# Optimization experiments

Hardware: AMD Instinct MI355X
Metric: run time of the kernel (lower is better)

The kernel has to match this reference:

```python
import jax, jax.numpy as jnp
import numpy as np

N_NODES = 25000
N_EDGES = 400000
EMBED_DIM = 128
NUM_HEADS = 8
D_K = EMBED_DIM // NUM_HEADS


def setup_inputs() -> dict:
    key = jax.random.key(0)
    ks = jax.random.split(key, 8)
    sc = 1.0 / np.sqrt(EMBED_DIM)
    return {
        "x": jax.random.normal(ks[0], (N_NODES, EMBED_DIM), jnp.float32),
        "edge_index": jax.random.randint(ks[1], (2, N_EDGES), 0, N_NODES),
        "attn_bias": jax.random.normal(ks[2], (N_EDGES, NUM_HEADS), jnp.float32),
        "Wq": jax.random.normal(ks[3], (EMBED_DIM, EMBED_DIM), jnp.float32) * sc,
        "bq": jnp.zeros((EMBED_DIM,), jnp.float32),
        "Wk": jax.random.normal(ks[4], (EMBED_DIM, EMBED_DIM), jnp.float32) * sc,
        "bk": jnp.zeros((EMBED_DIM,), jnp.float32),
        "Wv": jax.random.normal(ks[5], (EMBED_DIM, EMBED_DIM), jnp.float32) * sc,
        "bv": jnp.zeros((EMBED_DIM,), jnp.float32),
        "Wo": jax.random.normal(ks[6], (EMBED_DIM, EMBED_DIM), jnp.float32) * sc,
        "bo": jnp.zeros((EMBED_DIM,), jnp.float32),
    }


def reference(x, edge_index, attn_bias, Wq, bq, Wk, bk, Wv, bv, Wo, bo):
    N = x.shape[0]
    E = edge_index.shape[1]
    H, dk = NUM_HEADS, D_K
    scale = 1.0 / np.sqrt(dk).astype(np.float32)
    dst = edge_index[0]  # query/aggregation node per edge
    src = edge_index[1]  # key/value node per edge

    # project at node level (as torch: linear(x)[index]), then gather per edge
    q = (x @ Wq.T + bq)[dst].reshape(E, H, dk)
    k = (x @ Wk.T + bk)[src].reshape(E, H, dk)
    v = (x @ Wv.T + bv)[src].reshape(E, H, dk)

    logits = scale * jnp.sum(q * k, axis=2) + attn_bias  # [E, H]

    # segment softmax over edges grouped by destination node
    m = jax.ops.segment_max(logits, dst, num_segments=N)     # [N, H]
    e = jnp.exp(logits - m[dst])                              # [E, H]
    z = jax.ops.segment_sum(e, dst, num_segments=N)           # [N, H]
    scores = e / z[dst]                                       # [E, H]

    agg = jax.ops.segment_sum(scores[..., None] * v, dst, num_segments=N)  # [N, H, dk]
    out = agg.reshape(N, H * dk) @ Wo.T + bo                   # [N, embed_dim]
    return out, logits[..., None]
```

## Files before the change

### kernel.cpp

```cpp
#include <hip/hip_runtime.h>
#include <math.h>

#define N_NODES 25000
#define N_EDGES 400000
#define EMBED   128
#define HEADS   8
#define DK      16
#define MAXDEG  96
#define NX (N_NODES * 128)
#define SCAT_BLOCKS ((N_EDGES + 255) / 256)

typedef __attribute__((ext_vector_type(8))) short bf16x8;
typedef __attribute__((ext_vector_type(4))) float f32x4;
typedef unsigned int uint;
typedef unsigned short ushort;

__device__ inline uint pack2_bf16(float a, float b) {
    union { float f; uint u; } ua, ub;
    ua.f = a; ub.f = b;
    uint ra = (ua.u + 0x7FFFu + ((ua.u >> 16) & 1u)) >> 16;
    uint rb = (ub.u + 0x7FFFu + ((ub.u >> 16) & 1u)) >> 16;
    return (ra & 0xFFFFu) | (rb << 16);
}
__device__ inline ushort cvt_bf16(float a) {
    union { float f; uint u; } ua; ua.f = a;
    return (ushort)((ua.u + 0x7FFFu + ((ua.u >> 16) & 1u)) >> 16);
}
__device__ inline float bf16_lo(uint u) {
    union { uint u; float f; } x; x.u = u << 16; return x.f;
}
__device__ inline float bf16_hi(uint u) {
    union { uint u; float f; } x; x.u = u & 0xFFFF0000u; return x.f;
}

__global__ __launch_bounds__(256) void prep_scatter(
    const float* __restrict__ Wq, const float* __restrict__ Wk,
    const float* __restrict__ Wv, const float* __restrict__ Wo,
    ushort* __restrict__ wb,
    const int* __restrict__ ei, int* __restrict__ deg,
    int2* __restrict__ csr2)
{
    if (blockIdx.x < 128) {
        int i = blockIdx.x * 256 + threadIdx.x;
        int j = i * 2;
        const float* src = (j < 16384) ? Wq + j
                         : (j < 32768) ? Wk + (j - 16384)
                         : (j < 49152) ? Wv + (j - 32768)
                         :               Wo + (j - 49152);
        float2 v = *reinterpret_cast<const float2*>(src);
        reinterpret_cast<uint*>(wb)[i] = pack2_bf16(v.x, v.y);
    } else {
        int e = (blockIdx.x - 128) * 256 + threadIdx.x;
        if (e >= N_EDGES) return;
        int dst = ei[e];
        int src = ei[N_EDGES + e];
        int pos = atomicAdd(&deg[dst], 1);
        if (pos < MAXDEG) csr2[dst * MAXDEG + pos] = make_int2(e, src);
    }
}

__global__ __launch_bounds__(256) void gemm_qkv(
    const float* __restrict__ x, const ushort* __restrict__ Wall,
    const float* __restrict__ bq, const float* __restrict__ bk,
    const float* __restrict__ bv,
    ushort* __restrict__ Qb, ushort* __restrict__ Kb, ushort* __restrict__ Vb)
{
    const int which = blockIdx.y;
    const ushort* W = Wall + which * 16384;
    const float* bias = (which == 0) ? bq : (which == 1) ? bk : bv;
    ushort* C = (which == 0) ? Qb : (which == 1) ? Kb : Vb;

    const int lane = threadIdx.x & 63;
    const int wave = threadIdx.x >> 6;
    const int ml   = lane & 15;
    const int quad = lane >> 4;
    const int m0   = blockIdx.x * 64 + wave * 16;

    int arow = m0 + ml; if (arow >= N_NODES) arow = N_NODES - 1;
    const float* xp = x + arow * 128 + quad * 8;

    bf16x8 af[4];
#pragma unroll
    for (int ks = 0; ks < 4; ++ks) {
        float4 a0 = *reinterpret_cast<const float4*>(xp + ks * 32);
        float4 a1 = *reinterpret_cast<const float4*>(xp + ks * 32 + 4);
        uint* u = reinterpret_cast<uint*>(&af[ks]);
        u[0] = pack2_bf16(a0.x, a0.y); u[1] = pack2_bf16(a0.z, a0.w);
        u[2] = pack2_bf16(a1.x, a1.y); u[3] = pack2_bf16(a1.z, a1.w);
    }

    f32x4 acc[8];
#pragma unroll
    for (int ct = 0; ct < 8; ++ct) acc[ct] = (f32x4){0.f, 0.f, 0.f, 0.f};

#pragma unroll
    for (int ks = 0; ks < 4; ++ks) {
#pragma unroll
        for (int ct = 0; ct < 8; ++ct) {
            bf16x8 bf = *reinterpret_cast<const bf16x8*>(
                W + (ct * 16 + ml) * 128 + ks * 32 + quad * 8);
            acc[ct] = __builtin_amdgcn_mfma_f32_16x16x32_bf16(af[ks], bf, acc[ct], 0, 0, 0);
        }
    }

#pragma unroll
    for (int ct = 0; ct < 8; ++ct) {
        int col = ct * 16 + ml;
        float b = bias[col];
#pragma unroll
        for (int r = 0; r < 4; ++r) {
            int row = m0 + quad * 4 + r;
            if (row < N_NODES)
                C[row * 128 + col] = cvt_bf16(acc[ct][r] + b);
        }
    }
}

__global__ __launch_bounds__(256) void gemm_out(
    const ushort* __restrict__ A, const ushort* __restrict__ W,
    const float* __restrict__ bias, float* __restrict__ C, int M)
{
    const int lane = threadIdx.x & 63;
    const int wave = threadIdx.x >> 6;
    const int ml   = lane & 15;
    const int quad = lane >> 4;
    const int m0   = blockIdx.x * 64 + wave * 16;
    const int ct0  = blockIdx.y * 4;

    int arow = m0 + ml; if (arow >= M) arow = M - 1;
    const ushort* ap = A + arow * 128 + quad * 8;

    f32x4 acc[4];
#pragma unroll
    for (int ct = 0; ct < 4; ++ct) acc[ct] = (f32x4){0.f, 0.f, 0.f, 0.f};

#pragma unroll
    for (int ks = 0; ks < 128; ks += 32) {
        bf16x8 af = *reinterpret_cast<const bf16x8*>(ap + ks);
#pragma unroll
        for (int ct = 0; ct < 4; ++ct) {
            bf16x8 bf = *reinterpret_cast<const bf16x8*>(
                W + ((ct0 + ct) * 16 + ml) * 128 + ks + quad * 8);
            acc[ct] = __builtin_amdgcn_mfma_f32_16x16x32_bf16(af, bf, acc[ct], 0, 0, 0);
        }
    }

#pragma unroll
    for (int ct = 0; ct < 4; ++ct) {
        int col = (ct0 + ct) * 16 + ml;
        float bv_ = bias[col];
#pragma unroll
        for (int r = 0; r < 4; ++r) {
            int row = m0 + quad * 4 + r;
            if (row < M)
                C[row * 128 + col] = acc[ct][r] + bv_;
        }
    }
}

__global__ __launch_bounds__(256) void fused_attn(
    const ushort* __restrict__ Q2, const ushort* __restrict__ K2,
    const ushort* __restrict__ V2,
    const float* __restrict__ attn_bias,
    const int* __restrict__ deg, const int2* __restrict__ csr2,
    float* __restrict__ logits, ushort* __restrict__ AGG)
{
    const int lane = threadIdx.x & 63;
    const int wid  = threadIdx.x >> 6;
    const int n = blockIdx.x * 4 + wid;
    int dg = deg[n]; if (dg > MAXDEG) dg = MAXDEG;
    const int start = n * MAXDEG;
    const int h  = lane & 7;
    const int es = lane >> 3;

    const uint4* Qu4 = reinterpret_cast<const uint4*>(Q2);
    const uint4* Ku4 = reinterpret_cast<const uint4*>(K2);
    const uint4* Vu4 = reinterpret_cast<const uint4*>(V2);

    uint4 qa = Qu4[n * 16 + h * 2];
    uint4 qb = Qu4[n * 16 + h * 2 + 1];
    float qf[16];
    {
        uint qq[8] = {qa.x, qa.y, qa.z, qa.w, qb.x, qb.y, qb.z, qb.w};
#pragma unroll
        for (int j = 0; j < 8; ++j) {
            qf[2 * j]     = bf16_lo(qq[j]);
            qf[2 * j + 1] = bf16_hi(qq[j]);
        }
    }

    float acc[16];
#pragma unroll
    for (int j = 0; j < 16; ++j) acc[j] = 0.f;
    float z = 0.f;

    if (dg > 0) {
        int2 ep = csr2[start + (es < dg ? es : dg - 1)];
        for (int base = 0; base < dg; base += 8) {
            int e = ep.x, s = ep.y;
            bool valid = (base + es) < dg;

            uint4 k0 = Ku4[s * 16 + h * 2];
            uint4 k1 = Ku4[s * 16 + h * 2 + 1];
            uint4 v0 = Vu4[s * 16 + h * 2];
            uint4 v1 = Vu4[s * 16 + h * 2 + 1];
            float bias = attn_bias[e * 8 + h];

            int nb = base + 8;
            if (nb < dg) {
                int t2 = nb + es; if (t2 >= dg) t2 = dg - 1;
                ep = csr2[start + t2];
            }

            uint kk[8] = {k0.x, k0.y, k0.z, k0.w, k1.x, k1.y, k1.z, k1.w};
            float d = 0.f;
#pragma unroll
            for (int j = 0; j < 8; ++j)
                d += qf[2 * j] * bf16_lo(kk[j]) + qf[2 * j + 1] * bf16_hi(kk[j]);

            float l = 0.25f * d + bias;
            float p = 0.f;
            if (valid) {
                __builtin_nontemporal_store(l, &logits[e * 8 + h]);
                p = __expf(l);
            }
            z += p;

            uint vv[8] = {v0.x, v0.y, v0.z, v0.w, v1.x, v1.y, v1.z, v1.w};
#pragma unroll
            for (int j = 0; j < 8; ++j) {
                acc[2 * j]     += p * bf16_lo(vv[j]);
                acc[2 * j + 1] += p * bf16_hi(vv[j]);
            }
        }
    }

    {
        int bit = (lane >> 5) & 1;
#pragma unroll
        for (int j = 0; j < 8; ++j) {
            float send = bit ? acc[j] : acc[j + 8];
            float keep = bit ? acc[j + 8] : acc[j];
            acc[j] = keep + __shfl_xor(send, 32, 64);
        }
        bit = (lane >> 4) & 1;
#pragma unroll
        for (int j = 0; j < 4; ++j) {
            float send = bit ? acc[j] : acc[j + 4];
            float keep = bit ? acc[j + 4] : acc[j];
            acc[j] = keep + __shfl_xor(send, 16, 64);
        }
        bit = (lane >> 3) & 1;
#pragma unroll
        for (int j = 0; j < 2; ++j) {
            float send = bit ? acc[j] : acc[j + 2];
            float keep = bit ? acc[j + 2] : acc[j];
            acc[j] = keep + __shfl_xor(send, 8, 64);
        }
    }
    z += __shfl_xor(z, 8, 64);
    z += __shfl_xor(z, 16, 64);
    z += __shfl_xor(z, 32, 64);

    float inv = (z > 0.f) ? 1.f / z : 0.f;
    int d_off = ((lane >> 5) & 1) * 8 + ((lane >> 4) & 1) * 4 + ((lane >> 3) & 1) * 2;
    reinterpret_cast<uint*>(AGG)[n * 64 + h * 8 + (d_off >> 1)] =
        pack2_bf16(acc[0] * inv, acc[1] * inv);
}

extern "C" void kernel_launch(void* const* d_in, const int* in_sizes, int n_in,
                              void* d_out, int out_size, void* d_ws, size_t ws_size,
                              hipStream_t stream)
{
    const float* x         = (const float*)d_in[0];
    const int*   ei        = (const int*)  d_in[1];
    const float* attn_bias = (const float*)d_in[2];
    const float* Wq = (const float*)d_in[3];
    const float* bq = (const float*)d_in[4];
    const float* Wk = (const float*)d_in[5];
    const float* bk = (const float*)d_in[6];
    const float* Wv = (const float*)d_in[7];
    const float* bv = (const float*)d_in[8];
    const float* Wo = (const float*)d_in[9];
    const float* bo = (const float*)d_in[10];

    float* out    = (float*)d_out;
    float* logits = out + N_NODES * EMBED;

    ushort* wb   = (ushort*)d_ws;
    ushort* Qb   = wb + 4 * 16384;
    ushort* Kb   = Qb + NX;
    ushort* Vb   = Kb + NX;
    ushort* AGGb = Vb + NX;
    int* deg     = (int*)(AGGb + NX);
    int2* csr2   = (int2*)(deg + N_NODES);

    hipMemsetAsync(deg, 0, N_NODES * sizeof(int), stream);

    prep_scatter<<<128 + SCAT_BLOCKS, 256, 0, stream>>>(Wq, Wk, Wv, Wo, wb,
                                                        ei, deg, csr2);

    int gblocks = (N_NODES + 63) / 64;
    gemm_qkv<<<dim3(gblocks, 3), 256, 0, stream>>>(x, wb, bq, bk, bv, Qb, Kb, Vb);

    fused_attn<<<N_NODES / 4, 256, 0, stream>>>(Qb, Kb, Vb, attn_bias,
                                                deg, csr2, logits, AGGb);

    gemm_out<<<dim3(gblocks, 2), 256, 0, stream>>>(AGGb, wb + 3 * 16384, bo,
                                                   out, N_NODES);
}
```

Baseline: 198.5 us.

## Fuse edge scatter into QKV GEMM launch and fold degree zeroing into prep

Removes the hipMemsetAsync by zeroing the degree array inside the weight-conversion prep kernel. Moves the CSR edge scatter out of prep and into extra blocks of the QKV GEMM launch, so the scatter's atomics run alongside the GEMM blocks. Each scatter thread now handles four edges using vectorized int4 index loads. This saves one launch and lets the scatter overlap the projection, at the cost of a more heterogeneous kernel and edge-to-slot ordering that depends on atomic arrival order.

```diff
diff --git a/kernel.cpp b/kernel.cpp
--- a/kernel.cpp
+++ b/kernel.cpp
@@ -8,7 +8,8 @@
 #define DK      16
 #define MAXDEG  96
 #define NX (N_NODES * 128)
-#define SCAT_BLOCKS ((N_EDGES + 255) / 256)
+#define GBLK 391
+#define SCAT_BLK 391
 
 typedef __attribute__((ext_vector_type(8))) short bf16x8;
 typedef __attribute__((ext_vector_type(4))) float f32x4;
@@ -33,15 +34,14 @@
     union { uint u; float f; } x; x.u = u & 0xFFFF0000u; return x.f;
 }
 
-__global__ __launch_bounds__(256) void prep_scatter(
+__global__ __launch_bounds__(256) void prep(
     const float* __restrict__ Wq, const float* __restrict__ Wk,
     const float* __restrict__ Wv, const float* __restrict__ Wo,
-    ushort* __restrict__ wb,
-    const int* __restrict__ ei, int* __restrict__ deg,
-    int2* __restrict__ csr2)
-{
-    if (blockIdx.x < 128) {
-        int i = blockIdx.x * 256 + threadIdx.x;
+    ushort* __restrict__ wb, int* __restrict__ deg)
+{
+    int i = blockIdx.x * 256 + threadIdx.x;
+    if (i < N_NODES) deg[i] = 0;
+    if (i < 32768) {
         int j = i * 2;
         const float* src = (j < 16384) ? Wq + j
                          : (j < 32768) ? Wk + (j - 16384)
@@ -49,23 +49,37 @@
                          :               Wo + (j - 49152);
         float2 v = *reinterpret_cast<const float2*>(src);
         reinterpret_cast<uint*>(wb)[i] = pack2_bf16(v.x, v.y);
-    } else {
-        int e = (blockIdx.x - 128) * 256 + threadIdx.x;
-        if (e >= N_EDGES) return;
-        int dst = ei[e];
-        int src = ei[N_EDGES + e];
-        int pos = atomicAdd(&deg[dst], 1);
-        if (pos < MAXDEG) csr2[dst * MAXDEG + pos] = make_int2(e, src);
-    }
-}
-
-__global__ __launch_bounds__(256) void gemm_qkv(
+    }
+}
+
+__global__ __launch_bounds__(256) void gemm_qkv_scatter(
     const float* __restrict__ x, const ushort* __restrict__ Wall,
     const float* __restrict__ bq, const float* __restrict__ bk,
     const float* __restrict__ bv,
-    ushort* __restrict__ Qb, ushort* __restrict__ Kb, ushort* __restrict__ Vb)
-{
-    const int which = blockIdx.y;
+    ushort* __restrict__ Qb, ushort* __restrict__ Kb, ushort* __restrict__ Vb,
+    const int* __restrict__ ei, int* __restrict__ deg, int2* __restrict__ csr2)
+{
+    const int bx = blockIdx.x;
+    if (bx >= 3 * GBLK) {
+        int t = (bx - 3 * GBLK) * 256 + threadIdx.x;
+        int e = t * 4;
+        if (e < N_EDGES) {
+            int4 d = *reinterpret_cast<const int4*>(ei + e);
+            int4 s = *reinterpret_cast<const int4*>(ei + N_EDGES + e);
+            int p0 = atomicAdd(&deg[d.x], 1);
+            if (p0 < MAXDEG) csr2[d.x * MAXDEG + p0] = make_int2(e, s.x);
+            int p1 = atomicAdd(&deg[d.y], 1);
+            if (p1 < MAXDEG) csr2[d.y * MAXDEG + p1] = make_int2(e + 1, s.y);
+            int p2 = atomicAdd(&deg[d.z], 1);
+            if (p2 < MAXDEG) csr2[d.z * MAXDEG + p2] = make_int2(e + 2, s.z);
+            int p3 = atomicAdd(&deg[d.w], 1);
+            if (p3 < MAXDEG) csr2[d.w * MAXDEG + p3] = make_int2(e + 3, s.w);
+        }
+        return;
+    }
+
+    const int which = bx / GBLK;
+    const int mb    = bx - which * GBLK;
     const ushort* W = Wall + which * 16384;
     const float* bias = (which == 0) ? bq : (which == 1) ? bk : bv;
     ushort* C = (which == 0) ? Qb : (which == 1) ? Kb : Vb;
@@ -74,7 +88,7 @@
     const int wave = threadIdx.x >> 6;
     const int ml   = lane & 15;
     const int quad = lane >> 4;
-    const int m0   = blockIdx.x * 64 + wave * 16;
+    const int m0   = mb * 64 + wave * 16;
 
     int arow = m0 + ml; if (arow >= N_NODES) arow = N_NODES - 1;
     const float* xp = x + arow * 128 + quad * 8;
@@ -295,17 +309,14 @@
     int* deg     = (int*)(AGGb + NX);
     int2* csr2   = (int2*)(deg + N_NODES);
 
-    hipMemsetAsync(deg, 0, N_NODES * sizeof(int), stream);
-
-    prep_scatter<<<128 + SCAT_BLOCKS, 256, 0, stream>>>(Wq, Wk, Wv, Wo, wb,
-                                                        ei, deg, csr2);
-
-    int gblocks = (N_NODES + 63) / 64;
-    gemm_qkv<<<dim3(gblocks, 3), 256, 0, stream>>>(x, wb, bq, bk, bv, Qb, Kb, Vb);
+    prep<<<128, 256, 0, stream>>>(Wq, Wk, Wv, Wo, wb, deg);
+
+    gemm_qkv_scatter<<<3 * GBLK + SCAT_BLK, 256, 0, stream>>>(
+        x, wb, bq, bk, bv, Qb, Kb, Vb, ei, deg, csr2);
 
     fused_attn<<<N_NODES / 4, 256, 0, stream>>>(Qb, Kb, Vb, attn_bias,
                                                 deg, csr2, logits, AGGb);
 
-    gemm_out<<<dim3(gblocks, 2), 256, 0, stream>>>(AGGb, wb + 3 * 16384, bo,
-                                                   out, N_NODES);
-}
+    gemm_out<<<dim3(GBLK, 2), 256, 0, stream>>>(AGGb, wb + 3 * 16384, bo,
+                                                out, N_NODES);
+}
```

New measurement: 188.6 us. -5.0%, faster.
